# Optimization experiments

Hardware: AMD Instinct MI355X
Metric: run time of the kernel (lower is better)

## Reference

```python
import jax, jax.numpy as jnp
import numpy as np

N, D, M = 262144, 64, 256
CLAMP = -1e-9  # clamp_max value for the ray denominator


def setup_inputs() -> dict:
    key = jax.random.key(0)
    kz, kp, ka, kb = jax.random.split(key, 4)
    return {
        "z": jax.random.normal(kz, (N, D), dtype=jnp.float32),
        "pivot": jax.random.normal(kp, (D,), dtype=jnp.float32),
        "At": jax.random.normal(ka, (D, M), dtype=jnp.float32),
        "b": jax.random.normal(kb, (M,), dtype=jnp.float32),
    }


def reference(z, pivot, At, b):
    # sign_arg: [N, M] — signed constraint violation A z - b
    sign_arg = z @ At - b[None, :]
    ind = sign_arg >= 0  # violated constraints
    ray = pivot[None, :] - z  # [N, D] direction toward the interior pivot
    # denominator clamped to <= -1e-9 and detached (constant w.r.t. grads)
    denom = jax.lax.stop_gradient(jnp.minimum(ray @ At, CLAMP))  # [N, M]
    alpha = -sign_arg / denom
    # step size = max over violated constraints (alpha*ind zeros out satisfied ones)
    common_alpha = jnp.max(alpha * ind.astype(alpha.dtype), axis=1)  # [N]
    common_ind = jnp.any(ind, axis=1)  # [N] — move only if some constraint violated
    return z + common_ind[:, None].astype(z.dtype) * (common_alpha[:, None] * ray)
```

## Files before the change

### kernel.cpp

```cpp
#include <hip/hip_runtime.h>

#define DIMK 64
#define MC 256
#define BR 64
#define NROWS 262144
#define NT (NROWS / BR)
#define PB 512
#define TPB (NT / PB)

#define WS_AT 1024
#define WS_NEED (1024 + 65536)

#define LDS_AH 0
#define LDS_AL 16384
#define LDS_GM 32768
#define LDS_FB_SIZE 33280
#define LDS_GM3 65536
#define LDS_FP_SIZE 66560

typedef _Float16 half8 __attribute__((ext_vector_type(8)));
typedef float f32x16 __attribute__((ext_vector_type(16)));

__global__ void precompute_c(const float* __restrict__ pivot,
                             const float* __restrict__ At,
                             float* __restrict__ ws) {
    const int t = threadIdx.x;
    float acc = 0.f;
#pragma unroll
    for (int k = 0; k < DIMK; ++k) acc = fmaf(pivot[k], At[k * MC + t], acc);
    ws[t] = acc;
}

__global__ void precompute_at(const float* __restrict__ pivot,
                              const float* __restrict__ At,
                              float* __restrict__ ws) {
    const int t = threadIdx.x;
    float col[DIMK];
    float acc = 0.f;
#pragma unroll
    for (int k = 0; k < DIMK; ++k) {
        col[k] = At[k * MC + t];
        acc = fmaf(pivot[k], col[k], acc);
    }
    ws[t] = acc;
    char* wsb = (char*)ws + WS_AT;
#pragma unroll
    for (int s = 0; s < 2; ++s) {
#pragma unroll
        for (int kc = 0; kc < 4; ++kc) {
            half8 h, l;
#pragma unroll
            for (int j = 0; j < 8; ++j) {
                const float v = col[s * 32 + kc * 8 + j];
                h[j] = (_Float16)v;
                l[j] = (_Float16)(v - (float)h[j]);
            }
            const int off = ((s * 4 + kc) * 256 + t) * 16;
            *(half8*)(wsb + off) = h;
            *(half8*)(wsb + off + 32768) = l;
        }
    }
}

template <bool PREAT>
__global__ __launch_bounds__(256, 2)
void fused_constrain_mfma(const float* __restrict__ z,
                          const float* __restrict__ pivot,
                          const float* __restrict__ At,
                          const float* __restrict__ b,
                          const float* __restrict__ ws,
                          float* __restrict__ out) {
    extern __shared__ __align__(16) char lds[];

    const int tid  = threadIdx.x;
    const int lane = tid & 63;
    const int li   = lane & 31;
    const int hi   = lane >> 5;
    const int wid  = tid >> 6;
    const int rg   = wid >> 1;
    const int cg   = wid & 1;
    const int R0   = rg * 32;
    const int colbase = cg * 128;

    if constexpr (PREAT) {
        float bv[4], cv[4];
#pragma unroll
        for (int ct = 0; ct < 4; ++ct) {
            const int c = colbase + ct * 32 + li;
            bv[ct] = b[c];
            cv[ct] = ws[c];
        }
        const float2 p2 = *(const float2*)(pivot + 2 * li);

        float4 zfA[8], zfB[8];
        {
            const float* zr = z + blockIdx.x * (TPB * BR * DIMK) +
                              (R0 + li) * DIMK + hi * 8;
#pragma unroll
            for (int q = 0; q < 4; ++q) {
                const float* p = zr + (q >> 1) * 32 + (q & 1) * 16;
                zfA[q * 2 + 0] = *(const float4*)(p);
                zfA[q * 2 + 1] = *(const float4*)(p + 4);
            }
        }

        {
            const char* wsA = (const char*)ws + WS_AT;
#pragma unroll
            for (int p = 0; p < 16; ++p) {
                const int f = p * 256 + tid;
                *(float4*)(lds + f * 16) = *(const float4*)(wsA + f * 16);
            }
        }
        __syncthreads();

        const int Boff = hi * 4096 + (colbase + li) * 16;

        auto tile_body = [&](float4 (&zc)[8], float4 (&zn)[8],
                             const int i, const bool pf) {
            const int tbase = (blockIdx.x * TPB + i) * (BR * DIMK);

            if (pf) {
                const float* zr = z + tbase + BR * DIMK +
                                  (R0 + li) * DIMK + hi * 8;
#pragma unroll
                for (int q = 0; q < 4; ++q) {
                    const float* p = zr + (q >> 1) * 32 + (q & 1) * 16;
                    zn[q * 2 + 0] = *(const float4*)(p);
                    zn[q * 2 + 1] = *(const float4*)(p + 4);
                }
            }

            half8 azh[4], azl[4];
            const float* zv = (const float*)zc;
#pragma unroll
            for (int q = 0; q < 4; ++q)
#pragma unroll
                for (int j = 0; j < 8; ++j) {
                    const float v = zv[q * 8 + j];
                    azh[q][j] = (_Float16)v;
                    azl[q][j] = (_Float16)(v - (float)azh[q][j]);
                }

            f32x16 acc[4];
#pragma unroll
            for (int ct = 0; ct < 4; ++ct)
#pragma unroll
                for (int e = 0; e < 16; ++e) acc[ct][e] = 0.f;

#pragma unroll
            for (int s = 0; s < 2; ++s)
#pragma unroll
                for (int ksl = 0; ksl < 2; ++ksl) {
                    const half8 ah = azh[s * 2 + ksl], al = azl[s * 2 + ksl];
                    const int ob = Boff + s * 16384 + ksl * 8192;
#pragma unroll
                    for (int ct = 0; ct < 4; ++ct) {
                        const half8 bh = *(const half8*)(lds + ob + ct * 512);
                        const half8 bl = *(const half8*)(lds + ob + ct * 512 + 32768);
                        acc[ct] = __builtin_amdgcn_mfma_f32_32x32x16_f16(ah, bh, acc[ct], 0, 0, 0);
                        acc[ct] = __builtin_amdgcn_mfma_f32_32x32x16_f16(ah, bl, acc[ct], 0, 0, 0);
                        acc[ct] = __builtin_amdgcn_mfma_f32_32x32x16_f16(al, bh, acc[ct], 0, 0, 0);
                    }
                }

            float gm[16];
#pragma unroll
            for (int r = 0; r < 16; ++r) gm[r] = 0.f;
#pragma unroll
            for (int ct = 0; ct < 4; ++ct)
#pragma unroll
                for (int r = 0; r < 16; ++r) {
                    const float sv = acc[ct][r];
                    const float sa = sv - bv[ct];
                    const float qd = fmaxf(sv - cv[ct], 1e-9f);
                    gm[r] = fmaxf(gm[r], sa * __builtin_amdgcn_rcpf(qd));
                }
#pragma unroll
            for (int r = 0; r < 16; ++r)
#pragma unroll
                for (int off = 1; off < 32; off <<= 1)
                    gm[r] = fmaxf(gm[r], __shfl_xor(gm[r], off));

            float* gmb = (float*)(lds + LDS_GM3 + ((i & 1) << 9));
#pragma unroll
            for (int r = 0; r < 16; ++r) {
                const int row = (r & 3) + 8 * (r >> 2) + 4 * hi;
                if (li == 0) gmb[rg * 64 + row * 2 + cg] = gm[r];
            }
            __syncthreads();

            const int r0 = cg * 8;
#pragma unroll
            for (int rr = 0; rr < 8; ++rr) {
                const int r   = r0 + rr;
                const int row = (r & 3) + 8 * (r >> 2) + 4 * hi;
                const float g = fmaxf(gm[r], gmb[rg * 64 + row * 2 + (cg ^ 1)]);
                const int idx = tbase + (R0 + row) * DIMK + 2 * li;
                const float2 zz = *(const float2*)(z + idx);
                float2 o;
                o.x = fmaf(g, p2.x - zz.x, zz.x);
                o.y = fmaf(g, p2.y - zz.y, zz.y);
                *(float2*)(out + idx) = o;
            }
        };

#pragma clang loop unroll(disable)
        for (int j = 0; j < TPB / 2; ++j) {
            tile_body(zfA, zfB, 2 * j, true);
            tile_body(zfB, zfA, 2 * j + 1, j < TPB / 2 - 1);
        }
    } else {
        const int base = blockIdx.x * (BR * DIMK);
        float4 zf[8];
        {
            const float* zr = z + base + (R0 + li) * DIMK + hi * 8;
#pragma unroll
            for (int q = 0; q < 4; ++q) {
                const float* p = zr + (q >> 1) * 32 + (q & 1) * 16;
                zf[q * 2 + 0] = *(const float4*)(p);
                zf[q * 2 + 1] = *(const float4*)(p + 4);
            }
        }
        const int swzT = (tid & 3) ^ ((tid >> 2) & 3);
#pragma unroll
        for (int kc = 0; kc < 4; ++kc) {
            float v[8];
#pragma unroll
            for (int j = 0; j < 8; ++j) v[j] = At[(kc * 8 + j) * MC + tid];
            half8 h, l;
#pragma unroll
            for (int j = 0; j < 8; ++j) {
                h[j] = (_Float16)v[j];
                l[j] = (_Float16)(v[j] - (float)h[j]);
            }
            const int off = tid * 64 + ((kc ^ swzT) << 4);
            *(half8*)(lds + LDS_AH + off) = h;
            *(half8*)(lds + LDS_AL + off) = l;
        }

        half8 azh[4], azl[4];
        const float* zv = (const float*)zf;
#pragma unroll
        for (int q = 0; q < 4; ++q)
#pragma unroll
            for (int j = 0; j < 8; ++j) {
                const float v = zv[q * 8 + j];
                azh[q][j] = (_Float16)v;
                azl[q][j] = (_Float16)(v - (float)azh[q][j]);
            }

        f32x16 acc[4];
#pragma unroll
        for (int ct = 0; ct < 4; ++ct)
#pragma unroll
            for (int e = 0; e < 16; ++e) acc[ct][e] = 0.f;

        const int swz = (li & 3) ^ ((li >> 2) & 3);
        __syncthreads();
#pragma unroll
        for (int ksl = 0; ksl < 2; ++ksl) {
            const int cb = ((ksl * 2 + hi) ^ swz) << 4;
            const half8 ah = azh[ksl], al = azl[ksl];
#pragma unroll
            for (int ct = 0; ct < 4; ++ct) {
                const int off = (colbase + ct * 32 + li) * 64 + cb;
                const half8 bh = *(const half8*)(lds + LDS_AH + off);
                const half8 bl = *(const half8*)(lds + LDS_AL + off);
                acc[ct] = __builtin_amdgcn_mfma_f32_32x32x16_f16(ah, bh, acc[ct], 0, 0, 0);
                acc[ct] = __builtin_amdgcn_mfma_f32_32x32x16_f16(ah, bl, acc[ct], 0, 0, 0);
                acc[ct] = __builtin_amdgcn_mfma_f32_32x32x16_f16(al, bh, acc[ct], 0, 0, 0);
            }
        }
        __syncthreads();
#pragma unroll
        for (int kc = 0; kc < 4; ++kc) {
            float v[8];
#pragma unroll
            for (int j = 0; j < 8; ++j) v[j] = At[(32 + kc * 8 + j) * MC + tid];
            half8 h, l;
#pragma unroll
            for (int j = 0; j < 8; ++j) {
                h[j] = (_Float16)v[j];
                l[j] = (_Float16)(v[j] - (float)h[j]);
            }
            const int off = tid * 64 + ((kc ^ swzT) << 4);
            *(half8*)(lds + LDS_AH + off) = h;
            *(half8*)(lds + LDS_AL + off) = l;
        }
        __syncthreads();
#pragma unroll
        for (int ksl = 0; ksl < 2; ++ksl) {
            const int cb = ((ksl * 2 + hi) ^ swz) << 4;
            const half8 ah = azh[2 + ksl], al = azl[2 + ksl];
#pragma unroll
            for (int ct = 0; ct < 4; ++ct) {
                const int off = (colbase + ct * 32 + li) * 64 + cb;
                const half8 bh = *(const half8*)(lds + LDS_AH + off);
                const half8 bl = *(const half8*)(lds + LDS_AL + off);
                acc[ct] = __builtin_amdgcn_mfma_f32_32x32x16_f16(ah, bh, acc[ct], 0, 0, 0);
                acc[ct] = __builtin_amdgcn_mfma_f32_32x32x16_f16(ah, bl, acc[ct], 0, 0, 0);
                acc[ct] = __builtin_amdgcn_mfma_f32_32x32x16_f16(al, bh, acc[ct], 0, 0, 0);
            }
        }

        float bv[4], cv[4];
#pragma unroll
        for (int ct = 0; ct < 4; ++ct) {
            const int c = colbase + ct * 32 + li;
            bv[ct] = b[c];
            cv[ct] = ws[c];
        }
        float gm[16];
#pragma unroll
        for (int r = 0; r < 16; ++r) gm[r] = 0.f;
#pragma unroll
        for (int ct = 0; ct < 4; ++ct)
#pragma unroll
            for (int r = 0; r < 16; ++r) {
                const float sv = acc[ct][r];
                const float sa = sv - bv[ct];
                const float qd = fmaxf(sv - cv[ct], 1e-9f);
                gm[r] = fmaxf(gm[r], sa * __builtin_amdgcn_rcpf(qd));
            }
#pragma unroll
        for (int r = 0; r < 16; ++r)
#pragma unroll
            for (int off = 1; off < 32; off <<= 1)
                gm[r] = fmaxf(gm[r], __shfl_xor(gm[r], off));

        float* gmbuf = (float*)(lds + LDS_GM);
#pragma unroll
        for (int r = 0; r < 16; ++r) {
            const int row = (r & 3) + 8 * (r >> 2) + 4 * hi;
            if (li == 0) gmbuf[rg * 64 + row * 2 + cg] = gm[r];
        }
        __syncthreads();

        const float2 p2 = *(const float2*)(pivot + 2 * li);
        const int r0 = cg * 8;
#pragma unroll
        for (int rr = 0; rr < 8; ++rr) {
            const int r   = r0 + rr;
            const int row = (r & 3) + 8 * (r >> 2) + 4 * hi;
            const float g = fmaxf(gm[r], gmbuf[rg * 64 + row * 2 + (cg ^ 1)]);
            const int idx = base + (R0 + row) * DIMK + 2 * li;
            const float2 zz = *(const float2*)(z + idx);
            float2 o;
            o.x = fmaf(g, p2.x - zz.x, zz.x);
            o.y = fmaf(g, p2.y - zz.y, zz.y);
            *(float2*)(out + idx) = o;
        }
    }
}

extern "C" void kernel_launch(void* const* d_in, const int* in_sizes, int n_in,
                              void* d_out, int out_size, void* d_ws, size_t ws_size,
                              hipStream_t stream) {
    const float* z     = (const float*)d_in[0];
    const float* pivot = (const float*)d_in[1];
    const float* At    = (const float*)d_in[2];
    const float* b     = (const float*)d_in[3];
    float* ws = (float*)d_ws;
    if (ws_size >= (size_t)WS_NEED) {
        precompute_at<<<dim3(1), dim3(MC), 0, stream>>>(pivot, At, ws);
        fused_constrain_mfma<true><<<dim3(PB), dim3(256), LDS_FP_SIZE, stream>>>(
            z, pivot, At, b, ws, (float*)d_out);
    } else {
        precompute_c<<<dim3(1), dim3(MC), 0, stream>>>(pivot, At, ws);
        fused_constrain_mfma<false><<<dim3(NT), dim3(256), LDS_FB_SIZE, stream>>>(
            z, pivot, At, b, ws, (float*)d_out);
    }
}
```

Measured before the change: 156.9 us.

## Split persistent kernel across 8 waves with 64-column slices per wave

The persistent path now launches 512-thread blocks where each of eight waves owns 32 rows by 64 columns instead of 128 columns, halving per-wave accumulators and z registers. The second half of each z row is loaded inside the tile body instead of being prefetched with the first half, and the per-row max is combined across four column groups through LDS. This aims to raise occupancy and spread MFMA work over more waves, while adding extra LDS reduction traffic and less prefetch lookahead. The fallback kernel is split out into its own function using static shared memory.

```diff
diff --git a/kernel.cpp b/kernel.cpp
--- a/kernel.cpp
+++ b/kernel.cpp
@@ -5,21 +5,29 @@
 #define BR 64
 #define NROWS 262144
 #define NT (NROWS / BR)
-#define PB 512
-#define TPB (NT / PB)
+#define PBLK 512
+#define TPB (NT / PBLK)
 
 #define WS_AT 1024
 #define WS_NEED (1024 + 65536)
+
+#define LDS_GMP 65536
+#define LDS_FP_SIZE (65536 + 2048)
 
 #define LDS_AH 0
 #define LDS_AL 16384
 #define LDS_GM 32768
-#define LDS_FB_SIZE 33280
-#define LDS_GM3 65536
-#define LDS_FP_SIZE 66560
 
 typedef _Float16 half8 __attribute__((ext_vector_type(8)));
 typedef float f32x16 __attribute__((ext_vector_type(16)));
+
+__device__ __forceinline__ void cvt_half8(const float* v, half8& h, half8& l) {
+#pragma unroll
+    for (int j = 0; j < 8; ++j) {
+        h[j] = (_Float16)v[j];
+        l[j] = (_Float16)(v[j] - (float)h[j]);
+    }
+}
 
 __global__ void precompute_c(const float* __restrict__ pivot,
                              const float* __restrict__ At,
@@ -62,15 +70,161 @@
     }
 }
 
-template <bool PREAT>
-__global__ __launch_bounds__(256, 2)
-void fused_constrain_mfma(const float* __restrict__ z,
-                          const float* __restrict__ pivot,
-                          const float* __restrict__ At,
-                          const float* __restrict__ b,
-                          const float* __restrict__ ws,
-                          float* __restrict__ out) {
+__global__ __launch_bounds__(512, 4)
+void fused_constrain_p(const float* __restrict__ z,
+                       const float* __restrict__ pivot,
+                       const float* __restrict__ b,
+                       const float* __restrict__ ws,
+                       float* __restrict__ out) {
     extern __shared__ __align__(16) char lds[];
+
+    const int tid  = threadIdx.x;
+    const int lane = tid & 63;
+    const int li   = lane & 31;
+    const int hi   = lane >> 5;
+    const int wid  = tid >> 6;
+    const int rg   = wid >> 2;
+    const int cg   = wid & 3;
+    const int R0   = rg * 32;
+    const int colbase = cg * 64;
+
+    float bv[2], cv[2];
+#pragma unroll
+    for (int ct = 0; ct < 2; ++ct) {
+        const int c = colbase + ct * 32 + li;
+        bv[ct] = b[c];
+        cv[ct] = ws[c];
+    }
+    const float2 p2 = *(const float2*)(pivot + 2 * li);
+
+    float4 zfA[4];
+    {
+        const float* zr = z + blockIdx.x * (TPB * BR * DIMK) +
+                          (R0 + li) * DIMK + hi * 8;
+        zfA[0] = *(const float4*)(zr);
+        zfA[1] = *(const float4*)(zr + 4);
+        zfA[2] = *(const float4*)(zr + 16);
+        zfA[3] = *(const float4*)(zr + 20);
+    }
+
+    {
+        const char* wsA = (const char*)ws + WS_AT;
+#pragma unroll
+        for (int p = 0; p < 8; ++p) {
+            const int f = p * 512 + tid;
+            *(float4*)(lds + f * 16) = *(const float4*)(wsA + f * 16);
+        }
+    }
+    __syncthreads();
+
+    const int Bbase = hi * 4096 + (colbase + li) * 16;
+
+    auto tile_body = [&](float4 (&zc)[4], float4 (&zn)[4],
+                         const int i, const bool pf) {
+        const int tbase = (blockIdx.x * TPB + i) * (BR * DIMK);
+        const float* zr = z + tbase + (R0 + li) * DIMK + hi * 8;
+
+        float4 zs1[4];
+        zs1[0] = *(const float4*)(zr + 32);
+        zs1[1] = *(const float4*)(zr + 36);
+        zs1[2] = *(const float4*)(zr + 48);
+        zs1[3] = *(const float4*)(zr + 52);
+        if (pf) {
+            const float* zp = zr + BR * DIMK;
+            zn[0] = *(const float4*)(zp);
+            zn[1] = *(const float4*)(zp + 4);
+            zn[2] = *(const float4*)(zp + 16);
+            zn[3] = *(const float4*)(zp + 20);
+        }
+
+        f32x16 acc[2];
+#pragma unroll
+        for (int ct = 0; ct < 2; ++ct)
+#pragma unroll
+            for (int e = 0; e < 16; ++e) acc[ct][e] = 0.f;
+
+        half8 azh[2], azl[2];
+
+        auto mfma_step = [&](const int sOff) {
+#pragma unroll
+            for (int ksl = 0; ksl < 2; ++ksl) {
+                const int ob = Bbase + sOff + ksl * 8192;
+                const half8 ah = azh[ksl], al = azl[ksl];
+#pragma unroll
+                for (int ct = 0; ct < 2; ++ct) {
+                    const half8 bh = *(const half8*)(lds + ob + ct * 512);
+                    const half8 bl = *(const half8*)(lds + ob + ct * 512 + 32768);
+                    acc[ct] = __builtin_amdgcn_mfma_f32_32x32x16_f16(ah, bh, acc[ct], 0, 0, 0);
+                    acc[ct] = __builtin_amdgcn_mfma_f32_32x32x16_f16(ah, bl, acc[ct], 0, 0, 0);
+                    acc[ct] = __builtin_amdgcn_mfma_f32_32x32x16_f16(al, bh, acc[ct], 0, 0, 0);
+                }
+            }
+        };
+
+        cvt_half8((const float*)zc, azh[0], azl[0]);
+        cvt_half8((const float*)zc + 8, azh[1], azl[1]);
+        mfma_step(0);
+        cvt_half8((const float*)zs1, azh[0], azl[0]);
+        cvt_half8((const float*)zs1 + 8, azh[1], azl[1]);
+        mfma_step(16384);
+
+        float gm[16];
+#pragma unroll
+        for (int r = 0; r < 16; ++r) gm[r] = 0.f;
+#pragma unroll
+        for (int ct = 0; ct < 2; ++ct)
+#pragma unroll
+            for (int r = 0; r < 16; ++r) {
+                const float sv = acc[ct][r];
+                const float sa = sv - bv[ct];
+                const float qd = fmaxf(sv - cv[ct], 1e-9f);
+                gm[r] = fmaxf(gm[r], sa * __builtin_amdgcn_rcpf(qd));
+            }
+#pragma unroll
+        for (int r = 0; r < 16; ++r)
+#pragma unroll
+            for (int off = 1; off < 32; off <<= 1)
+                gm[r] = fmaxf(gm[r], __shfl_xor(gm[r], off));
+
+        float* gmb = (float*)(lds + LDS_GMP + ((i & 1) << 10));
+#pragma unroll
+        for (int r = 0; r < 16; ++r) {
+            const int row = (r & 3) + 8 * (r >> 2) + 4 * hi;
+            if (li == 0) gmb[((rg << 5) + row) * 4 + cg] = gm[r];
+        }
+        __syncthreads();
+
+#pragma unroll
+        for (int rr = 0; rr < 4; ++rr) {
+            const int r   = cg * 4 + rr;
+            const int row = (r & 3) + 8 * (r >> 2) + 4 * hi;
+            const float* g4 = &gmb[((rg << 5) + row) * 4];
+            const float g = fmaxf(fmaxf(g4[0], g4[1]), fmaxf(g4[2], g4[3]));
+            const int idx = tbase + (R0 + row) * DIMK + 2 * li;
+            const float2 zz = *(const float2*)(z + idx);
+            float2 o;
+            o.x = fmaf(g, p2.x - zz.x, zz.x);
+            o.y = fmaf(g, p2.y - zz.y, zz.y);
+            *(float2*)(out + idx) = o;
+        }
+    };
+
+    float4 zfB[4];
+#pragma clang loop unroll(disable)
+    for (int j = 0; j < TPB / 2; ++j) {
+        tile_body(zfA, zfB, 2 * j, true);
+        tile_body(zfB, zfA, 2 * j + 1, j < TPB / 2 - 1);
+    }
+}
+
+__global__ __launch_bounds__(256, 4)
+void fused_constrain_fb(const float* __restrict__ z,
+                        const float* __restrict__ pivot,
+                        const float* __restrict__ At,
+                        const float* __restrict__ b,
+                        const float* __restrict__ ws,
+                        float* __restrict__ out) {
+    __shared__ __align__(16) char lds[33280];
 
     const int tid  = threadIdx.x;
     const int lane = tid & 63;
@@ -81,276 +235,141 @@
     const int cg   = wid & 1;
     const int R0   = rg * 32;
     const int colbase = cg * 128;
-
-    if constexpr (PREAT) {
-        float bv[4], cv[4];
+    const int base = blockIdx.x * (BR * DIMK);
+
+    float4 zf[8];
+    {
+        const float* zr = z + base + (R0 + li) * DIMK + hi * 8;
+#pragma unroll
+        for (int q = 0; q < 4; ++q) {
+            const float* p = zr + (q >> 1) * 32 + (q & 1) * 16;
+            zf[q * 2 + 0] = *(const float4*)(p);
+            zf[q * 2 + 1] = *(const float4*)(p + 4);
+        }
+    }
+    const int swzT = (tid & 3) ^ ((tid >> 2) & 3);
+#pragma unroll
+    for (int kc = 0; kc < 4; ++kc) {
+        float v[8];
+#pragma unroll
+        for (int j = 0; j < 8; ++j) v[j] = At[(kc * 8 + j) * MC + tid];
+        half8 h, l;
+#pragma unroll
+        for (int j = 0; j < 8; ++j) {
+            h[j] = (_Float16)v[j];
+            l[j] = (_Float16)(v[j] - (float)h[j]);
+        }
+        const int off = tid * 64 + ((kc ^ swzT) << 4);
+        *(half8*)(lds + LDS_AH + off) = h;
+        *(half8*)(lds + LDS_AL + off) = l;
+    }
+
+    half8 azh[4], azl[4];
+    const float* zv = (const float*)zf;
+#pragma unroll
+    for (int q = 0; q < 4; ++q)
+        cvt_half8(zv + q * 8, azh[q], azl[q]);
+
+    f32x16 acc[4];
+#pragma unroll
+    for (int ct = 0; ct < 4; ++ct)
+#pragma unroll
+        for (int e = 0; e < 16; ++e) acc[ct][e] = 0.f;
+
+    const int swz = (li & 3) ^ ((li >> 2) & 3);
+    __syncthreads();
+#pragma unroll
+    for (int ksl = 0; ksl < 2; ++ksl) {
+        const int cb = ((ksl * 2 + hi) ^ swz) << 4;
+        const half8 ah = azh[ksl], al = azl[ksl];
 #pragma unroll
         for (int ct = 0; ct < 4; ++ct) {
-            const int c = colbase + ct * 32 + li;
-            bv[ct] = b[c];
-            cv[ct] = ws[c];
-        }
-        const float2 p2 = *(const float2*)(pivot + 2 * li);
-
-        float4 zfA[8], zfB[8];
-        {
-            const float* zr = z + blockIdx.x * (TPB * BR * DIMK) +
-                              (R0 + li) * DIMK + hi * 8;
-#pragma unroll
-            for (int q = 0; q < 4; ++q) {
-                const float* p = zr + (q >> 1) * 32 + (q & 1) * 16;
-                zfA[q * 2 + 0] = *(const float4*)(p);
-                zfA[q * 2 + 1] = *(const float4*)(p + 4);
-            }
-        }
-
-        {
-            const char* wsA = (const char*)ws + WS_AT;
-#pragma unroll
-            for (int p = 0; p < 16; ++p) {
-                const int f = p * 256 + tid;
-                *(float4*)(lds + f * 16) = *(const float4*)(wsA + f * 16);
-            }
-        }
-        __syncthreads();
-
-        const int Boff = hi * 4096 + (colbase + li) * 16;
-
-        auto tile_body = [&](float4 (&zc)[8], float4 (&zn)[8],
-                             const int i, const bool pf) {
-            const int tbase = (blockIdx.x * TPB + i) * (BR * DIMK);
-
-            if (pf) {
-                const float* zr = z + tbase + BR * DIMK +
-                                  (R0 + li) * DIMK + hi * 8;
-#pragma unroll
-                for (int q = 0; q < 4; ++q) {
-                    const float* p = zr + (q >> 1) * 32 + (q & 1) * 16;
-                    zn[q * 2 + 0] = *(const float4*)(p);
-                    zn[q * 2 + 1] = *(const float4*)(p + 4);
-                }
-            }
-
-            half8 azh[4], azl[4];
-            const float* zv = (const float*)zc;
-#pragma unroll
-            for (int q = 0; q < 4; ++q)
-#pragma unroll
-                for (int j = 0; j < 8; ++j) {
-                    const float v = zv[q * 8 + j];
-                    azh[q][j] = (_Float16)v;
-                    azl[q][j] = (_Float16)(v - (float)azh[q][j]);
-                }
-
-            f32x16 acc[4];
-#pragma unroll
-            for (int ct = 0; ct < 4; ++ct)
-#pragma unroll
-                for (int e = 0; e < 16; ++e) acc[ct][e] = 0.f;
-
-#pragma unroll
-            for (int s = 0; s < 2; ++s)
-#pragma unroll
-                for (int ksl = 0; ksl < 2; ++ksl) {
-                    const half8 ah = azh[s * 2 + ksl], al = azl[s * 2 + ksl];
-                    const int ob = Boff + s * 16384 + ksl * 8192;
-#pragma unroll
-                    for (int ct = 0; ct < 4; ++ct) {
-                        const half8 bh = *(const half8*)(lds + ob + ct * 512);
-                        const half8 bl = *(const half8*)(lds + ob + ct * 512 + 32768);
-                        acc[ct] = __builtin_amdgcn_mfma_f32_32x32x16_f16(ah, bh, acc[ct], 0, 0, 0);
-                        acc[ct] = __builtin_amdgcn_mfma_f32_32x32x16_f16(ah, bl, acc[ct], 0, 0, 0);
-                        acc[ct] = __builtin_amdgcn_mfma_f32_32x32x16_f16(al, bh, acc[ct], 0, 0, 0);
-                    }
-                }
-
-            float gm[16];
-#pragma unroll
-            for (int r = 0; r < 16; ++r) gm[r] = 0.f;
-#pragma unroll
-            for (int ct = 0; ct < 4; ++ct)
-#pragma unroll
-                for (int r = 0; r < 16; ++r) {
-                    const float sv = acc[ct][r];
-                    const float sa = sv - bv[ct];
-                    const float qd = fmaxf(sv - cv[ct], 1e-9f);
-                    gm[r] = fmaxf(gm[r], sa * __builtin_amdgcn_rcpf(qd));
-                }
-#pragma unroll
-            for (int r = 0; r < 16; ++r)
-#pragma unroll
-                for (int off = 1; off < 32; off <<= 1)
-                    gm[r] = fmaxf(gm[r], __shfl_xor(gm[r], off));
-
-            float* gmb = (float*)(lds + LDS_GM3 + ((i & 1) << 9));
-#pragma unroll
-            for (int r = 0; r < 16; ++r) {
-                const int row = (r & 3) + 8 * (r >> 2) + 4 * hi;
-                if (li == 0) gmb[rg * 64 + row * 2 + cg] = gm[r];
-            }
-            __syncthreads();
-
-            const int r0 = cg * 8;
-#pragma unroll
-            for (int rr = 0; rr < 8; ++rr) {
-                const int r   = r0 + rr;
-                const int row = (r & 3) + 8 * (r >> 2) + 4 * hi;
-                const float g = fmaxf(gm[r], gmb[rg * 64 + row * 2 + (cg ^ 1)]);
-                const int idx = tbase + (R0 + row) * DIMK + 2 * li;
-                const float2 zz = *(const float2*)(z + idx);
-                float2 o;
-                o.x = fmaf(g, p2.x - zz.x, zz.x);
-                o.y = fmaf(g, p2.y - zz.y, zz.y);
-                *(float2*)(out + idx) = o;
-            }
-        };
-
-#pragma clang loop unroll(disable)
-        for (int j = 0; j < TPB / 2; ++j) {
-            tile_body(zfA, zfB, 2 * j, true);
-            tile_body(zfB, zfA, 2 * j + 1, j < TPB / 2 - 1);
-        }
-    } else {
-        const int base = blockIdx.x * (BR * DIMK);
-        float4 zf[8];
-        {
-            const float* zr = z + base + (R0 + li) * DIMK + hi * 8;
-#pragma unroll
-            for (int q = 0; q < 4; ++q) {
-                const float* p = zr + (q >> 1) * 32 + (q & 1) * 16;
-                zf[q * 2 + 0] = *(const float4*)(p);
-                zf[q * 2 + 1] = *(const float4*)(p + 4);
-            }
-        }
-        const int swzT = (tid & 3) ^ ((tid >> 2) & 3);
-#pragma unroll
-        for (int kc = 0; kc < 4; ++kc) {
-            float v[8];
-#pragma unroll
-            for (int j = 0; j < 8; ++j) v[j] = At[(kc * 8 + j) * MC + tid];
-            half8 h, l;
-#pragma unroll
-            for (int j = 0; j < 8; ++j) {
-                h[j] = (_Float16)v[j];
-                l[j] = (_Float16)(v[j] - (float)h[j]);
-            }
-            const int off = tid * 64 + ((kc ^ swzT) << 4);
-            *(half8*)(lds + LDS_AH + off) = h;
-            *(half8*)(lds + LDS_AL + off) = l;
-        }
-
-        half8 azh[4], azl[4];
-        const float* zv = (const float*)zf;
-#pragma unroll
-        for (int q = 0; q < 4; ++q)
-#pragma unroll
-            for (int j = 0; j < 8; ++j) {
-                const float v = zv[q * 8 + j];
-                azh[q][j] = (_Float16)v;
-                azl[q][j] = (_Float16)(v - (float)azh[q][j]);
-            }
-
-        f32x16 acc[4];
-#pragma unroll
-        for (int ct = 0; ct < 4; ++ct)
-#pragma unroll
-            for (int e = 0; e < 16; ++e) acc[ct][e] = 0.f;
-
-        const int swz = (li & 3) ^ ((li >> 2) & 3);
-        __syncthreads();
-#pragma unroll
-        for (int ksl = 0; ksl < 2; ++ksl) {
-            const int cb = ((ksl * 2 + hi) ^ swz) << 4;
-            const half8 ah = azh[ksl], al = azl[ksl];
-#pragma unroll
-            for (int ct = 0; ct < 4; ++ct) {
-                const int off = (colbase + ct * 32 + li) * 64 + cb;
-                const half8 bh = *(const half8*)(lds + LDS_AH + off);
-                const half8 bl = *(const half8*)(lds + LDS_AL + off);
-                acc[ct] = __builtin_amdgcn_mfma_f32_32x32x16_f16(ah, bh, acc[ct], 0, 0, 0);
-                acc[ct] = __builtin_amdgcn_mfma_f32_32x32x16_f16(ah, bl, acc[ct], 0, 0, 0);
-                acc[ct] = __builtin_amdgcn_mfma_f32_32x32x16_f16(al, bh, acc[ct], 0, 0, 0);
-            }
-        }
-        __syncthreads();
-#pragma unroll
-        for (int kc = 0; kc < 4; ++kc) {
-            float v[8];
-#pragma unroll
-            for (int j = 0; j < 8; ++j) v[j] = At[(32 + kc * 8 + j) * MC + tid];
-            half8 h, l;
-#pragma unroll
-            for (int j = 0; j < 8; ++j) {
-                h[j] = (_Float16)v[j];
-                l[j] = (_Float16)(v[j] - (float)h[j]);
-            }
-            const int off = tid * 64 + ((kc ^ swzT) << 4);
-            *(half8*)(lds + LDS_AH + off) = h;
-            *(half8*)(lds + LDS_AL + off) = l;
-        }
-        __syncthreads();
-#pragma unroll
-        for (int ksl = 0; ksl < 2; ++ksl) {
-            const int cb = ((ksl * 2 + hi) ^ swz) << 4;
-            const half8 ah = azh[2 + ksl], al = azl[2 + ksl];
-#pragma unroll
-            for (int ct = 0; ct < 4; ++ct) {
-                const int off = (colbase + ct * 32 + li) * 64 + cb;
-                const half8 bh = *(const half8*)(lds + LDS_AH + off);
-                const half8 bl = *(const half8*)(lds + LDS_AL + off);
-                acc[ct] = __builtin_amdgcn_mfma_f32_32x32x16_f16(ah, bh, acc[ct], 0, 0, 0);
-                acc[ct] = __builtin_amdgcn_mfma_f32_32x32x16_f16(ah, bl, acc[ct], 0, 0, 0);
-                acc[ct] = __builtin_amdgcn_mfma_f32_32x32x16_f16(al, bh, acc[ct], 0, 0, 0);
-            }
-        }
-
-        float bv[4], cv[4];
+            const int off = (colbase + ct * 32 + li) * 64 + cb;
+            const half8 bh = *(const half8*)(lds + LDS_AH + off);
+            const half8 bl = *(const half8*)(lds + LDS_AL + off);
+            acc[ct] = __builtin_amdgcn_mfma_f32_32x32x16_f16(ah, bh, acc[ct], 0, 0, 0);
+            acc[ct] = __builtin_amdgcn_mfma_f32_32x32x16_f16(ah, bl, acc[ct], 0, 0, 0);
+            acc[ct] = __builtin_amdgcn_mfma_f32_32x32x16_f16(al, bh, acc[ct], 0, 0, 0);
+        }
+    }
+    __syncthreads();
+#pragma unroll
+    for (int kc = 0; kc < 4; ++kc) {
+        float v[8];
+#pragma unroll
+        for (int j = 0; j < 8; ++j) v[j] = At[(32 + kc * 8 + j) * MC + tid];
+        half8 h, l;
+#pragma unroll
+        for (int j = 0; j < 8; ++j) {
+            h[j] = (_Float16)v[j];
+            l[j] = (_Float16)(v[j] - (float)h[j]);
+        }
+        const int off = tid * 64 + ((kc ^ swzT) << 4);
+        *(half8*)(lds + LDS_AH + off) = h;
+        *(half8*)(lds + LDS_AL + off) = l;
+    }
+    __syncthreads();
+#pragma unroll
+    for (int ksl = 0; ksl < 2; ++ksl) {
+        const int cb = ((ksl * 2 + hi) ^ swz) << 4;
+        const half8 ah = azh[2 + ksl], al = azl[2 + ksl];
 #pragma unroll
         for (int ct = 0; ct < 4; ++ct) {
-            const int c = colbase + ct * 32 + li;
-            bv[ct] = b[c];
-            cv[ct] = ws[c];
-        }
-        float gm[16];
-#pragma unroll
-        for (int r = 0; r < 16; ++r) gm[r] = 0.f;
-#pragma unroll
-        for (int ct = 0; ct < 4; ++ct)
-#pragma unroll
-            for (int r = 0; r < 16; ++r) {
-                const float sv = acc[ct][r];
-                const float sa = sv - bv[ct];
-                const float qd = fmaxf(sv - cv[ct], 1e-9f);
-                gm[r] = fmaxf(gm[r], sa * __builtin_amdgcn_rcpf(qd));
-            }
-#pragma unroll
-        for (int r = 0; r < 16; ++r)
-#pragma unroll
-            for (int off = 1; off < 32; off <<= 1)
-                gm[r] = fmaxf(gm[r], __shfl_xor(gm[r], off));
-
-        float* gmbuf = (float*)(lds + LDS_GM);
+            const int off = (colbase + ct * 32 + li) * 64 + cb;
+            const half8 bh = *(const half8*)(lds + LDS_AH + off);
+            const half8 bl = *(const half8*)(lds + LDS_AL + off);
+            acc[ct] = __builtin_amdgcn_mfma_f32_32x32x16_f16(ah, bh, acc[ct], 0, 0, 0);
+            acc[ct] = __builtin_amdgcn_mfma_f32_32x32x16_f16(ah, bl, acc[ct], 0, 0, 0);
+            acc[ct] = __builtin_amdgcn_mfma_f32_32x32x16_f16(al, bh, acc[ct], 0, 0, 0);
+        }
+    }
+
+    float bv[4], cv[4];
+#pragma unroll
+    for (int ct = 0; ct < 4; ++ct) {
+        const int c = colbase + ct * 32 + li;
+        bv[ct] = b[c];
+        cv[ct] = ws[c];
+    }
+    float gm[16];
+#pragma unroll
+    for (int r = 0; r < 16; ++r) gm[r] = 0.f;
+#pragma unroll
+    for (int ct = 0; ct < 4; ++ct)
 #pragma unroll
         for (int r = 0; r < 16; ++r) {
-            const int row = (r & 3) + 8 * (r >> 2) + 4 * hi;
-            if (li == 0) gmbuf[rg * 64 + row * 2 + cg] = gm[r];
-        }
-        __syncthreads();
-
-        const float2 p2 = *(const float2*)(pivot + 2 * li);
-        const int r0 = cg * 8;
-#pragma unroll
-        for (int rr = 0; rr < 8; ++rr) {
-            const int r   = r0 + rr;
-            const int row = (r & 3) + 8 * (r >> 2) + 4 * hi;
-            const float g = fmaxf(gm[r], gmbuf[rg * 64 + row * 2 + (cg ^ 1)]);
-            const int idx = base + (R0 + row) * DIMK + 2 * li;
-            const float2 zz = *(const float2*)(z + idx);
-            float2 o;
-            o.x = fmaf(g, p2.x - zz.x, zz.x);
-            o.y = fmaf(g, p2.y - zz.y, zz.y);
-            *(float2*)(out + idx) = o;
-        }
+            const float sv = acc[ct][r];
+            const float sa = sv - bv[ct];
+            const float qd = fmaxf(sv - cv[ct], 1e-9f);
+            gm[r] = fmaxf(gm[r], sa * __builtin_amdgcn_rcpf(qd));
+        }
+#pragma unroll
+    for (int r = 0; r < 16; ++r)
+#pragma unroll
+        for (int off = 1; off < 32; off <<= 1)
+            gm[r] = fmaxf(gm[r], __shfl_xor(gm[r], off));
+
+    float* gmbuf = (float*)(lds + LDS_GM);
+#pragma unroll
+    for (int r = 0; r < 16; ++r) {
+        const int row = (r & 3) + 8 * (r >> 2) + 4 * hi;
+        if (li == 0) gmbuf[rg * 64 + row * 2 + cg] = gm[r];
+    }
+    __syncthreads();
+
+    const float2 p2 = *(const float2*)(pivot + 2 * li);
+    const int r0 = cg * 8;
+#pragma unroll
+    for (int rr = 0; rr < 8; ++rr) {
+        const int r   = r0 + rr;
+        const int row = (r & 3) + 8 * (r >> 2) + 4 * hi;
+        const float g = fmaxf(gm[r], gmbuf[rg * 64 + row * 2 + (cg ^ 1)]);
+        const int idx = base + (R0 + row) * DIMK + 2 * li;
+        const float2 zz = *(const float2*)(z + idx);
+        float2 o;
+        o.x = fmaf(g, p2.x - zz.x, zz.x);
+        o.y = fmaf(g, p2.y - zz.y, zz.y);
+        *(float2*)(out + idx) = o;
     }
 }
 
@@ -364,11 +383,11 @@
     float* ws = (float*)d_ws;
     if (ws_size >= (size_t)WS_NEED) {
         precompute_at<<<dim3(1), dim3(MC), 0, stream>>>(pivot, At, ws);
-        fused_constrain_mfma<true><<<dim3(PB), dim3(256), LDS_FP_SIZE, stream>>>(
-            z, pivot, At, b, ws, (float*)d_out);
+        fused_constrain_p<<<dim3(PBLK), dim3(512), LDS_FP_SIZE, stream>>>(
+            z, pivot, b, ws, (float*)d_out);
     } else {
         precompute_c<<<dim3(1), dim3(MC), 0, stream>>>(pivot, At, ws);
-        fused_constrain_mfma<false><<<dim3(NT), dim3(256), LDS_FB_SIZE, stream>>>(
+        fused_constrain_fb<<<dim3(NT), dim3(256), 0, stream>>>(
             z, pivot, At, b, ws, (float*)d_out);
     }
 }
```

After: 158.2 us. About the same (+0.9%).
